# Performance work log

Hardware: AMD Instinct MI355X
Metric: run time of the kernel (lower is better)

Reference implementation:

```python
import jax, jax.numpy as jnp
from jax import lax
import numpy as np

C = 768      # embed_dim
H = 8        # num_heads
SR = 2       # sr_ratio
EPS = 1e-5


def setup_inputs() -> dict:
    key = jax.random.key(0)
    ks = jax.random.split(key, 8)
    B, n = 1, 24
    N = n ** 3  # 13824
    s = 0.02
    x = jax.random.normal(ks[0], (B, N, C), jnp.float32)
    wq = jax.random.normal(ks[1], (C, C), jnp.float32) * s          # query (no bias)
    wkv = jax.random.normal(ks[2], (C, 2 * C), jnp.float32) * s     # key_value (no bias)
    sr_w = jax.random.normal(ks[3], (C, C, SR, SR, SR), jnp.float32) * s  # Conv3d OIDHW
    sr_b = jax.random.normal(ks[4], (C,), jnp.float32) * s
    ln_g = jnp.ones((C,), jnp.float32)
    ln_b = jnp.zeros((C,), jnp.float32)
    proj_w = jax.random.normal(ks[5], (C, C), jnp.float32) * s
    proj_b = jax.random.normal(ks[6], (C,), jnp.float32) * s
    return {"x": x, "wq": wq, "wkv": wkv, "sr_w": sr_w, "sr_b": sr_b,
            "ln_g": ln_g, "ln_b": ln_b, "proj_w": proj_w, "proj_b": proj_b}


def reference(x, wq, wkv, sr_w, sr_b, ln_g, ln_b, proj_w, proj_b):
    B, N, Cdim = x.shape
    d = Cdim // H
    n = round(N ** (1.0 / 3.0))
    # q: [B,H,N,d]
    q = (x @ wq).reshape(B, N, H, d).transpose(0, 2, 1, 3)
    # spatial reduction: conv3d with kernel=stride=SR
    x_ = x.transpose(0, 2, 1).reshape(B, Cdim, n, n, n)
    x_ = lax.conv_general_dilated(x_, sr_w, (SR, SR, SR), 'VALID',
                                  dimension_numbers=('NCDHW', 'OIDHW', 'NCDHW'))
    x_ = x_ + sr_b[None, :, None, None, None]
    x_ = x_.reshape(B, Cdim, -1).transpose(0, 2, 1)  # [B, N', C]
    mu = x_.mean(-1, keepdims=True)
    var = x_.var(-1, keepdims=True)
    x_ = (x_ - mu) / jnp.sqrt(var + EPS) * ln_g + ln_b
    # kv: [2,B,H,N',d]
    kv = (x_ @ wkv).reshape(B, -1, 2, H, d).transpose(2, 0, 3, 1, 4)
    k, v = kv[0], kv[1]
    # NOTE: original scales by sqrt(num_heads), not sqrt(head_dim) -- kept faithfully.
    scores = jnp.einsum('bhqd,bhkd->bhqk', q, k) / jnp.sqrt(jnp.float32(H))
    probs = jax.nn.softmax(scores, axis=-1)
    out = jnp.einsum('bhqk,bhkd->bhqd', probs, v)
    out = out.transpose(0, 2, 1, 3).reshape(B, N, Cdim)
    return out @ proj_w + proj_b
```

## Files before the change

kernel.cpp:

```cpp
#include <hip/hip_runtime.h>
#include <hip/hip_bf16.h>

typedef __hip_bfloat16 bf16;
typedef unsigned short u16;

#define CD 768
#define HH 8
#define HD 96
#define NT 13824
#define NR 1728
#define KCONV 6144

typedef __attribute__((ext_vector_type(8))) __bf16 bf16x8;
typedef __attribute__((ext_vector_type(8))) unsigned short us8;
typedef __attribute__((ext_vector_type(4))) unsigned short us4;
typedef __attribute__((ext_vector_type(4))) float floatx4;

#define OFF_XB   0L
#define OFF_Q    21233664L
#define OFF_XR   42467328L
#define OFF_XLN  47775744L
#define OFF_WQT  50429952L
#define OFF_WKVT 51609600L
#define OFF_PRJT 53968896L
#define OFF_SRWR 55148544L
#define OFF_PRB  64587264L
#define OFF_FLAG 64588800L

__device__ __forceinline__ float b2f(bf16 v) { return __bfloat162float(v); }
__device__ __forceinline__ floatx4 mfma16(bf16x8 a, bf16x8 b, floatx4 c) {
    return __builtin_amdgcn_mfma_f32_16x16x32_bf16(a, b, c, 0, 0, 0);
}
__device__ __forceinline__ u16 f2bf_bits(float x) {
    return __builtin_bit_cast(u16, __float2bfloat16(x));
}
__device__ __forceinline__ float ldin(const void* p, long i, int bf) {
    return bf ? b2f(((const bf16*)p)[i]) : ((const float*)p)[i];
}

__global__ void detect_kernel(const unsigned short* __restrict__ g, int* __restrict__ flag) {
    *flag = (g[0] == 0x3F80) ? 1 : 0;
}

__global__ __launch_bounds__(256) void cvt_kernel(
    const void* __restrict__ src, bf16* __restrict__ dst, long nchunk,
    const int* __restrict__ flagp)
{
    const int bf = *flagp;
    long c = (long)blockIdx.x * 256 + threadIdx.x;
    if (c >= nchunk) return;
    if (bf) {
        ((us8*)dst)[c] = ((const us8*)src)[c];
    } else {
        const float* s = (const float*)src + c * 8;
        us8 o;
#pragma unroll
        for (int j = 0; j < 8; ++j) o[j] = f2bf_bits(s[j]);
        ((us8*)dst)[c] = o;
    }
}

__global__ __launch_bounds__(256) void trans_kernel(
    const void* __restrict__ src, bf16* __restrict__ dst, int R, int Cc,
    const int* __restrict__ flagp)
{
    const int bf = *flagp;
    __shared__ float tile[32][33];
    const int tx = threadIdx.x & 31, ty = threadIdx.x >> 5;
    const int bx = blockIdx.x * 32, by = blockIdx.y * 32;
#pragma unroll
    for (int rr = 0; rr < 4; ++rr)
        tile[ty + rr * 8][tx] = ldin(src, (long)(by + ty + rr * 8) * Cc + bx + tx, bf);
    __syncthreads();
#pragma unroll
    for (int rr = 0; rr < 4; ++rr)
        dst[(long)(bx + ty + rr * 8) * R + by + tx] =
            __float2bfloat16(tile[tx][ty + rr * 8]);
}

__global__ __launch_bounds__(256) void reorder_srw_kernel(
    const void* __restrict__ src, bf16* __restrict__ dst,
    const int* __restrict__ flagp)
{
    const int bf = *flagp;
    const long total = 768L * 6144;
    for (long e = (long)blockIdx.x * 256 + threadIdx.x; e < total;
         e += (long)gridDim.x * 256) {
        long o = e / 6144;
        int rem = (int)(e - o * 6144);
        int tap = rem / 768, i = rem - tap * 768;
        dst[e] = __float2bfloat16(ldin(src, o * 6144 + i * 8 + tap, bf));
    }
}

template <bool GATHER, bool BIAS, int DST, int SPLITK, bool PRESCALE>
__global__ __launch_bounds__(256) void gemm_mfma(
    const bf16* __restrict__ A, const bf16* __restrict__ Bt,
    const bf16* __restrict__ bias, void* __restrict__ C, bf16* __restrict__ C2,
    int M, int N, int K, const int* __restrict__ flagp)
{
    const int bf = (DST == 0) ? *flagp : 0;
    __shared__ u16 Al[128][40];
    __shared__ u16 Bl[128][40];
    const int tid  = threadIdx.x;
    const int wave = tid >> 6, lane = tid & 63;
    const int l15  = lane & 15, quad = lane >> 4;
    const int m0 = blockIdx.y * 128, n0 = blockIdx.x * 128;
    const int mw = (wave & 1) * 64, nw = (wave >> 1) * 64;
    const int srow = tid >> 1, koff = (tid & 1) * 16;

    const int mclamp = min(m0 + srow, M - 1);
    int tokbase = 0;
    if (GATHER) {
        int zo = mclamp / 144, yo = (mclamp / 12) % 12, xo = mclamp % 12;
        tokbase = zo * 1152 + yo * 48 + xo * 2;
    }
    const long arow_off = (long)mclamp * K;
    const long brow_off = (long)(n0 + srow) * K;

    floatx4 acc[4][4];
#pragma unroll
    for (int mi = 0; mi < 4; ++mi)
#pragma unroll
        for (int ni = 0; ni < 4; ++ni) acc[mi][ni] = (floatx4){0.f, 0.f, 0.f, 0.f};

    const int ksteps = K >> 5;
    const int kchunk = ksteps / SPLITK;
    const int kb0 = (SPLITK > 1) ? blockIdx.z * kchunk : 0;
    const int kbend = kb0 + kchunk;

    us8 a0, a1, b0, b1;
    {
        const bf16* asrc;
        if (GATHER) {
            int kk0 = kb0 << 5;
            int tap = kk0 / 768;
            int i0  = kk0 - tap * 768 + koff;
            int tok = tokbase + (tap >> 2) * 576 + ((tap >> 1) & 1) * 24 + (tap & 1);
            asrc = A + (long)tok * 768 + i0;
        } else {
            asrc = A + arow_off + (kb0 << 5) + koff;
        }
        a0 = *(const us8*)asrc;
        a1 = *(const us8*)(asrc + 8);
        b0 = *(const us8*)(Bt + brow_off + (kb0 << 5) + koff);
        b1 = *(const us8*)(Bt + brow_off + (kb0 << 5) + koff + 8);
    }

    for (int kb = kb0; kb < kbend; ++kb) {
        __syncthreads();
        *(us8*)&Al[srow][koff]     = a0;
        *(us8*)&Al[srow][koff + 8] = a1;
        *(us8*)&Bl[srow][koff]     = b0;
        *(us8*)&Bl[srow][koff + 8] = b1;
        __syncthreads();

        if (kb + 1 < kbend) {
            const int kn = kb + 1;
            const bf16* asrc;
            if (GATHER) {
                int kk0 = kn << 5;
                int tap = kk0 / 768;
                int i0  = kk0 - tap * 768 + koff;
                int tok = tokbase + (tap >> 2) * 576 + ((tap >> 1) & 1) * 24 + (tap & 1);
                asrc = A + (long)tok * 768 + i0;
            } else {
                asrc = A + arow_off + (kn << 5) + koff;
            }
            a0 = *(const us8*)asrc;
            a1 = *(const us8*)(asrc + 8);
            b0 = *(const us8*)(Bt + brow_off + (kn << 5) + koff);
            b1 = *(const us8*)(Bt + brow_off + (kn << 5) + koff + 8);
        }

        bf16x8 af[4], bfr[4];
#pragma unroll
        for (int mi = 0; mi < 4; ++mi)
            af[mi] = *(const bf16x8*)&Al[mw + mi * 16 + l15][quad * 8];
#pragma unroll
        for (int ni = 0; ni < 4; ++ni)
            bfr[ni] = *(const bf16x8*)&Bl[nw + ni * 16 + l15][quad * 8];
#pragma unroll
        for (int mi = 0; mi < 4; ++mi)
#pragma unroll
            for (int ni = 0; ni < 4; ++ni)
                acc[mi][ni] = mfma16(af[mi], bfr[ni], acc[mi][ni]);
    }

#pragma unroll
    for (int mi = 0; mi < 4; ++mi) {
        int rowb = m0 + mw + mi * 16 + quad * 4;
#pragma unroll
        for (int ni = 0; ni < 4; ++ni) {
            int col = n0 + nw + ni * 16 + l15;
            float bv = BIAS ? b2f(bias[col]) : 0.f;
#pragma unroll
            for (int r = 0; r < 4; ++r) {
                int row = rowb + r;
                if (row < M) {
                    float v = acc[mi][ni][r] + bv;
                    if (PRESCALE) v *= 0.35355339059327373f;
                    long idx = (long)row * N + col;
                    if (DST == 2)      ((float*)C)[idx] = v;
                    else if (DST == 1) ((bf16*)C)[idx] = __float2bfloat16(v);
                    else if (DST == 3) {
                        if (col < 768) ((bf16*)C)[(long)row * 768 + col] = __float2bfloat16(v);
                        else           C2[(long)(col - 768) * NR + row] = __float2bfloat16(v);
                    } else if (DST == 4) {
                        atomicAdd((float*)C + idx, v);
                    } else {
                        if (bf) ((bf16*)C)[idx] = __float2bfloat16(v);
                        else    ((float*)C)[idx] = v;
                    }
                }
            }
        }
    }
}

__global__ __launch_bounds__(256) void ln_kernel(
    const float* __restrict__ Xr, const void* __restrict__ srb,
    const void* __restrict__ g, const void* __restrict__ b,
    bf16* __restrict__ Xln, const int* __restrict__ flagp)
{
    const int bf = *flagp;
    __shared__ float red[256];
    __shared__ float mu_s, rs_s;
    const int t = blockIdx.x, tid = threadIdx.x;
    const float* row = Xr + (long)t * CD;
    float v0 = row[tid]       + ldin(srb, tid, bf);
    float v1 = row[tid + 256] + ldin(srb, tid + 256, bf);
    float v2 = row[tid + 512] + ldin(srb, tid + 512, bf);
    red[tid] = v0 + v1 + v2;
    __syncthreads();
    for (int off = 128; off; off >>= 1) {
        if (tid < off) red[tid] += red[tid + off];
        __syncthreads();
    }
    if (tid == 0) mu_s = red[0] * (1.0f / CD);
    __syncthreads();
    float mu = mu_s;
    float d0 = v0 - mu, d1 = v1 - mu, d2 = v2 - mu;
    red[tid] = d0 * d0 + d1 * d1 + d2 * d2;
    __syncthreads();
    for (int off = 128; off; off >>= 1) {
        if (tid < off) red[tid] += red[tid + off];
        __syncthreads();
    }
    if (tid == 0) rs_s = rsqrtf(red[0] * (1.0f / CD) + 1e-5f);
    __syncthreads();
    float rs = rs_s;
    bf16* orow = Xln + (long)t * CD;
    orow[tid]       = __float2bfloat16(d0 * rs * ldin(g, tid, bf)       + ldin(b, tid, bf));
    orow[tid + 256] = __float2bfloat16(d1 * rs * ldin(g, tid + 256, bf) + ldin(b, tid + 256, bf));
    orow[tid + 512] = __float2bfloat16(d2 * rs * ldin(g, tid + 512, bf) + ldin(b, tid + 512, bf));
}

__global__ __launch_bounds__(256, 2) void attn_mfma_kernel(
    const bf16* __restrict__ Qg, const bf16* __restrict__ Kg,
    const bf16* __restrict__ VTg, bf16* __restrict__ Og)
{
    __shared__ u16 Ks[64][104];
    __shared__ u16 Vt[96][72];
    __shared__ u16 PT[4][64][72];

    const int tid  = threadIdx.x;
    const int wave = tid >> 6;
    const int lane = tid & 63;
    const int l15  = lane & 15;
    const int quad = lane >> 4;

    const int lin  = blockIdx.y * 54 + blockIdx.x;
    const int nid  = (lin & 7) * 54 + (lin >> 3);
    const int h    = nid / 54;
    const int qblk = nid - h * 54;
    const int q0   = qblk * 256 + wave * 64;

    bf16x8 bq[4][3];
#pragma unroll
    for (int qc = 0; qc < 4; ++qc)
#pragma unroll
        for (int kc = 0; kc < 3; ++kc)
            bq[qc][kc] = *(const bf16x8*)(Qg + (long)(q0 + qc * 16 + l15) * CD
                                          + h * HD + kc * 32 + quad * 8);

    floatx4 o[4][6];
    float lp[4] = {0.f, 0.f, 0.f, 0.f};
#pragma unroll
    for (int qc = 0; qc < 4; ++qc)
#pragma unroll
        for (int dc = 0; dc < 6; ++dc) o[qc][dc] = (floatx4){0.f, 0.f, 0.f, 0.f};

    const int stok = tid >> 2;
    const int dseg = (tid & 3) * 24;
    const int vdim = tid >> 3;
    const int vt8  = (tid & 7) << 3;
    const u16* kbase = (const u16*)Kg + (long)stok * 768 + h * HD + dseg;
    const u16* vbase = (const u16*)VTg + (long)(h * HD + vdim) * NR + vt8;

    us8 kreg[3], vreg[3];
#pragma unroll
    for (int s = 0; s < 3; ++s) kreg[s] = *(const us8*)(kbase + s * 8);
#pragma unroll
    for (int i = 0; i < 3; ++i) vreg[i] = *(const us8*)(vbase + (long)i * 32 * NR);

    for (int kt = 0; kt < NR; kt += 64) {
        __syncthreads();
#pragma unroll
        for (int s = 0; s < 3; ++s) *(us8*)&Ks[stok][dseg + s * 8] = kreg[s];
#pragma unroll
        for (int i = 0; i < 3; ++i) *(us8*)&Vt[vdim + i * 32][vt8] = vreg[i];
        __syncthreads();

        if (kt + 64 < NR) {
            const u16* k2 = kbase + (long)(kt + 64) * 768;
            const u16* v2 = vbase + (kt + 64);
#pragma unroll
            for (int s = 0; s < 3; ++s) kreg[s] = *(const us8*)(k2 + s * 8);
#pragma unroll
            for (int i = 0; i < 3; ++i) vreg[i] = *(const us8*)(v2 + (long)i * 32 * NR);
        }

#pragma unroll
        for (int tc = 0; tc < 4; ++tc) {
            bf16x8 ak[3];
#pragma unroll
            for (int kc = 0; kc < 3; ++kc)
                ak[kc] = *(const bf16x8*)&Ks[tc * 16 + l15][kc * 32 + quad * 8];
#pragma unroll
            for (int qc = 0; qc < 4; ++qc) {
                floatx4 acc = {0.f, 0.f, 0.f, 0.f};
#pragma unroll
                for (int kc = 0; kc < 3; ++kc) acc = mfma16(ak[kc], bq[qc][kc], acc);
                float e0 = __expf(acc[0]), e1 = __expf(acc[1]);
                float e2 = __expf(acc[2]), e3 = __expf(acc[3]);
                lp[qc] += (e0 + e1) + (e2 + e3);
                us4 p4;
                p4[0] = f2bf_bits(e0); p4[1] = f2bf_bits(e1);
                p4[2] = f2bf_bits(e2); p4[3] = f2bf_bits(e3);
                *(us4*)&PT[wave][qc * 16 + l15][tc * 16 + quad * 4] = p4;
            }
        }

#pragma unroll
        for (int ks = 0; ks < 2; ++ks) {
            bf16x8 ap[4];
#pragma unroll
            for (int qc = 0; qc < 4; ++qc)
                ap[qc] = *(const bf16x8*)&PT[wave][qc * 16 + l15][ks * 32 + quad * 8];
#pragma unroll
            for (int dc = 0; dc < 6; ++dc) {
                bf16x8 bv = *(const bf16x8*)&Vt[dc * 16 + l15][ks * 32 + quad * 8];
#pragma unroll
                for (int qc = 0; qc < 4; ++qc)
                    o[qc][dc] = mfma16(ap[qc], bv, o[qc][dc]);
            }
        }
    }

#pragma unroll
    for (int qc = 0; qc < 4; ++qc) {
        float ls = lp[qc];
        ls += __shfl_xor(ls, 16);
        ls += __shfl_xor(ls, 32);
        float inv = 1.0f / ls;
#pragma unroll
        for (int r = 0; r < 4; ++r) {
            float invr = __shfl(inv, quad * 4 + r, 16);
            int row = q0 + qc * 16 + quad * 4 + r;
#pragma unroll
            for (int dc = 0; dc < 6; ++dc)
                Og[(long)row * CD + h * HD + dc * 16 + l15] =
                    __float2bfloat16(o[qc][dc][r] * invr);
        }
    }
}

extern "C" void kernel_launch(void* const* d_in, const int* in_sizes, int n_in,
                              void* d_out, int out_size, void* d_ws, size_t ws_size,
                              hipStream_t stream) {
    const void* x      = d_in[0];
    const void* wq     = d_in[1];
    const void* wkv    = d_in[2];
    const void* sr_w   = d_in[3];
    const void* sr_b   = d_in[4];
    const void* ln_g   = d_in[5];
    const void* ln_b   = d_in[6];
    const void* proj_w = d_in[7];
    const void* proj_b = d_in[8];

    char* ws = (char*)d_ws;
    bf16*  xb    = (bf16*)(ws + OFF_XB);
    bf16*  O     = (bf16*)(ws + OFF_XB);
    bf16*  Q     = (bf16*)(ws + OFF_Q);
    float* Xr    = (float*)(ws + OFF_XR);
    bf16*  Kg    = (bf16*)(ws + OFF_XR);
    bf16*  VTg   = (bf16*)(ws + OFF_XR + 2654208);
    bf16*  Xln   = (bf16*)(ws + OFF_XLN);
    bf16*  wqT   = (bf16*)(ws + OFF_WQT);
    bf16*  wkvT  = (bf16*)(ws + OFF_WKVT);
    bf16*  prjT  = (bf16*)(ws + OFF_PRJT);
    bf16*  srwR  = (bf16*)(ws + OFF_SRWR);
    bf16*  prbB  = (bf16*)(ws + OFF_PRB);
    int*   flag  = (int*)(ws + OFF_FLAG);

    detect_kernel<<<1, 1, 0, stream>>>((const unsigned short*)ln_g, flag);
    cvt_kernel<<<5184, 256, 0, stream>>>(x, xb, (long)NT * CD / 8, flag);
    trans_kernel<<<dim3(24, 24), 256, 0, stream>>>(wq, wqT, CD, CD, flag);
    trans_kernel<<<dim3(48, 24), 256, 0, stream>>>(wkv, wkvT, CD, 1536, flag);
    trans_kernel<<<dim3(24, 24), 256, 0, stream>>>(proj_w, prjT, CD, CD, flag);
    reorder_srw_kernel<<<4608, 256, 0, stream>>>(sr_w, srwR, flag);
    cvt_kernel<<<1, 256, 0, stream>>>(proj_b, prbB, CD / 8, flag);

    hipMemsetAsync(Xr, 0, (long)NR * CD * 4, stream);
    gemm_mfma<true, false, 4, 4, false><<<dim3(6, 14, 4), 256, 0, stream>>>(
        xb, srwR, nullptr, Xr, nullptr, NR, CD, KCONV, flag);
    ln_kernel<<<NR, 256, 0, stream>>>(Xr, sr_b, ln_g, ln_b, Xln, flag);
    gemm_mfma<false, false, 3, 1, false><<<dim3(12, 14), 256, 0, stream>>>(
        Xln, wkvT, nullptr, Kg, VTg, NR, 1536, CD, flag);
    gemm_mfma<false, false, 1, 1, true><<<dim3(6, 108), 256, 0, stream>>>(
        xb, wqT, nullptr, Q, nullptr, NT, CD, CD, flag);
    attn_mfma_kernel<<<dim3(NT / 256, HH), 256, 0, stream>>>(Q, Kg, VTg, O);
    gemm_mfma<false, true, 0, 1, false><<<dim3(6, 108), 256, 0, stream>>>(
        O, prjT, prbB, d_out, nullptr, NT, CD, CD, flag);
}
```

Baseline: 406.1 us.

## Use direct global-to-LDS loads with double buffering and swizzle in GEMM

The GEMM staging moves from register-staged loads to global_load_lds writes straight into a double-buffered, XOR-swizzled LDS tile without padding, and drops one barrier per k-step. The goal is to overlap the next tile's fetch with the current MFMA work and cut register pressure and LDS bank conflicts. The attention kernel also raises wave priority around its MFMA blocks with s_setprio. The main risk is correctness of the swizzle mapping for global_load_lds lane layout, since each lane writes a fixed 16-byte slot per wave.

```diff
diff --git a/kernel.cpp b/kernel.cpp
--- a/kernel.cpp
+++ b/kernel.cpp
@@ -38,6 +38,10 @@
     return bf ? b2f(((const bf16*)p)[i]) : ((const float*)p)[i];
 }
 
+#define GLOAD16(gp, lp) __builtin_amdgcn_global_load_lds( \
+    (const __attribute__((address_space(1))) unsigned int*)(gp), \
+    (__attribute__((address_space(3))) unsigned int*)(lp), 16, 0, 0)
+
 __global__ void detect_kernel(const unsigned short* __restrict__ g, int* __restrict__ flag) {
     *flag = (g[0] == 0x3F80) ? 1 : 0;
 }
@@ -100,23 +104,35 @@
     int M, int N, int K, const int* __restrict__ flagp)
 {
     const int bf = (DST == 0) ? *flagp : 0;
-    __shared__ u16 Al[128][40];
-    __shared__ u16 Bl[128][40];
+    __shared__ alignas(16) u16 Al[2][128][32];
+    __shared__ alignas(16) u16 Bl[2][128][32];
     const int tid  = threadIdx.x;
     const int wave = tid >> 6, lane = tid & 63;
     const int l15  = lane & 15, quad = lane >> 4;
     const int m0 = blockIdx.y * 128, n0 = blockIdx.x * 128;
     const int mw = (wave & 1) * 64, nw = (wave >> 1) * 64;
-    const int srow = tid >> 1, koff = (tid & 1) * 16;
-
-    const int mclamp = min(m0 + srow, M - 1);
-    int tokbase = 0;
-    if (GATHER) {
-        int zo = mclamp / 144, yo = (mclamp / 12) % 12, xo = mclamp % 12;
-        tokbase = zo * 1152 + yo * 48 + xo * 2;
-    }
-    const long arow_off = (long)mclamp * K;
-    const long brow_off = (long)(n0 + srow) * K;
+
+    const int row0 = wave * 16 + (lane >> 2);
+    const int row1 = row0 + 64;
+    const int cb8  = (((lane & 3) ^ ((lane >> 3) & 3)) << 3);
+
+    int tokbase0 = 0, tokbase1 = 0;
+    long arow0 = 0, arow1 = 0;
+    {
+        int mc0 = min(m0 + row0, M - 1);
+        int mc1 = min(m0 + row1, M - 1);
+        if (GATHER) {
+            int zo0 = mc0 / 144, yo0 = (mc0 / 12) % 12, xo0 = mc0 % 12;
+            tokbase0 = zo0 * 1152 + yo0 * 48 + xo0 * 2;
+            int zo1 = mc1 / 144, yo1 = (mc1 / 12) % 12, xo1 = mc1 % 12;
+            tokbase1 = zo1 * 1152 + yo1 * 48 + xo1 * 2;
+        } else {
+            arow0 = (long)mc0 * K;
+            arow1 = (long)mc1 * K;
+        }
+    }
+    const long brow0 = (long)(n0 + row0) * K;
+    const long brow1 = (long)(n0 + row1) * K;
 
     floatx4 acc[4][4];
 #pragma unroll
@@ -129,62 +145,51 @@
     const int kb0 = (SPLITK > 1) ? blockIdx.z * kchunk : 0;
     const int kbend = kb0 + kchunk;
 
-    us8 a0, a1, b0, b1;
-    {
-        const bf16* asrc;
+    auto stage = [&](int kb, int c) {
+        const long ko = (long)kb << 5;
+        const bf16 *ga0, *ga1;
         if (GATHER) {
-            int kk0 = kb0 << 5;
+            int kk0 = kb << 5;
             int tap = kk0 / 768;
-            int i0  = kk0 - tap * 768 + koff;
-            int tok = tokbase + (tap >> 2) * 576 + ((tap >> 1) & 1) * 24 + (tap & 1);
-            asrc = A + (long)tok * 768 + i0;
+            int i0  = kk0 - tap * 768 + cb8;
+            int toff = (tap >> 2) * 576 + ((tap >> 1) & 1) * 24 + (tap & 1);
+            ga0 = A + (long)(tokbase0 + toff) * 768 + i0;
+            ga1 = A + (long)(tokbase1 + toff) * 768 + i0;
         } else {
-            asrc = A + arow_off + (kb0 << 5) + koff;
-        }
-        a0 = *(const us8*)asrc;
-        a1 = *(const us8*)(asrc + 8);
-        b0 = *(const us8*)(Bt + brow_off + (kb0 << 5) + koff);
-        b1 = *(const us8*)(Bt + brow_off + (kb0 << 5) + koff + 8);
-    }
+            ga0 = A + arow0 + ko + cb8;
+            ga1 = A + arow1 + ko + cb8;
+        }
+        GLOAD16(ga0, &Al[c][wave * 16][0]);
+        GLOAD16(ga1, &Al[c][64 + wave * 16][0]);
+        GLOAD16(Bt + brow0 + ko + cb8, &Bl[c][wave * 16][0]);
+        GLOAD16(Bt + brow1 + ko + cb8, &Bl[c][64 + wave * 16][0]);
+    };
+
+    int cur = 0;
+    stage(kb0, 0);
+    asm volatile("s_waitcnt vmcnt(0)" ::: "memory");
+    __syncthreads();
+
+    const int sl = ((quad ^ ((l15 >> 1) & 3)) << 3);
 
     for (int kb = kb0; kb < kbend; ++kb) {
-        __syncthreads();
-        *(us8*)&Al[srow][koff]     = a0;
-        *(us8*)&Al[srow][koff + 8] = a1;
-        *(us8*)&Bl[srow][koff]     = b0;
-        *(us8*)&Bl[srow][koff + 8] = b1;
-        __syncthreads();
-
-        if (kb + 1 < kbend) {
-            const int kn = kb + 1;
-            const bf16* asrc;
-            if (GATHER) {
-                int kk0 = kn << 5;
-                int tap = kk0 / 768;
-                int i0  = kk0 - tap * 768 + koff;
-                int tok = tokbase + (tap >> 2) * 576 + ((tap >> 1) & 1) * 24 + (tap & 1);
-                asrc = A + (long)tok * 768 + i0;
-            } else {
-                asrc = A + arow_off + (kn << 5) + koff;
-            }
-            a0 = *(const us8*)asrc;
-            a1 = *(const us8*)(asrc + 8);
-            b0 = *(const us8*)(Bt + brow_off + (kn << 5) + koff);
-            b1 = *(const us8*)(Bt + brow_off + (kn << 5) + koff + 8);
-        }
-
+        if (kb + 1 < kbend) stage(kb + 1, cur ^ 1);
         bf16x8 af[4], bfr[4];
 #pragma unroll
         for (int mi = 0; mi < 4; ++mi)
-            af[mi] = *(const bf16x8*)&Al[mw + mi * 16 + l15][quad * 8];
+            af[mi] = *(const bf16x8*)&Al[cur][mw + mi * 16 + l15][sl];
 #pragma unroll
         for (int ni = 0; ni < 4; ++ni)
-            bfr[ni] = *(const bf16x8*)&Bl[nw + ni * 16 + l15][quad * 8];
+            bfr[ni] = *(const bf16x8*)&Bl[cur][nw + ni * 16 + l15][sl];
 #pragma unroll
         for (int mi = 0; mi < 4; ++mi)
 #pragma unroll
             for (int ni = 0; ni < 4; ++ni)
                 acc[mi][ni] = mfma16(af[mi], bfr[ni], acc[mi][ni]);
+
+        asm volatile("s_waitcnt vmcnt(0)" ::: "memory");
+        __syncthreads();
+        cur ^= 1;
     }
 
 #pragma unroll
@@ -330,8 +335,10 @@
 #pragma unroll
             for (int qc = 0; qc < 4; ++qc) {
                 floatx4 acc = {0.f, 0.f, 0.f, 0.f};
+                __builtin_amdgcn_s_setprio(1);
 #pragma unroll
                 for (int kc = 0; kc < 3; ++kc) acc = mfma16(ak[kc], bq[qc][kc], acc);
+                __builtin_amdgcn_s_setprio(0);
                 float e0 = __expf(acc[0]), e1 = __expf(acc[1]);
                 float e2 = __expf(acc[2]), e3 = __expf(acc[3]);
                 lp[qc] += (e0 + e1) + (e2 + e3);
@@ -348,6 +355,7 @@
 #pragma unroll
             for (int qc = 0; qc < 4; ++qc)
                 ap[qc] = *(const bf16x8*)&PT[wave][qc * 16 + l15][ks * 32 + quad * 8];
+            __builtin_amdgcn_s_setprio(1);
 #pragma unroll
             for (int dc = 0; dc < 6; ++dc) {
                 bf16x8 bv = *(const bf16x8*)&Vt[dc * 16 + l15][ks * 32 + quad * 8];
@@ -355,6 +363,7 @@
                 for (int qc = 0; qc < 4; ++qc)
                     o[qc][dc] = mfma16(ap[qc], bv, o[qc][dc]);
             }
+            __builtin_amdgcn_s_setprio(0);
         }
     }
 
```

Result: faster. 392.4 us (-3.4%).
